# Optimization experiments

Measured on AMD Instinct MI355X. Metric: run time of the kernel, lower is better.

Reference implementation:

```python
import jax, jax.numpy as jnp
import numpy as np

L1, L2, B, D1, D2, HEADS, M = 1024, 1024, 8, 512, 1024, 16, 1024
DPH = M // HEADS  # 64


def setup_inputs() -> dict:
    key = jax.random.key(0)
    ks = jax.random.split(key, 10)
    w = lambda k, shp: jax.random.normal(k, shp, jnp.float32) * 0.02
    z = lambda n: jnp.zeros((n,), jnp.float32)
    return {
        "ctx_1": jax.random.normal(ks[0], (L1, B, D1), jnp.float32),
        "ctx_2": jax.random.normal(ks[1], (L2, B, D2), jnp.float32),
        "Wk1": w(ks[2], (M, D1)), "bk1": z(M),
        "Wv1": w(ks[3], (M, D1)), "bv1": z(M),
        "Wk2": w(ks[4], (M, D2)), "bk2": z(M),
        "Wv2": w(ks[5], (M, D2)), "bv2": z(M),
        "Wf12": w(ks[6], (M, M)), "bf12": z(M),
        "Wf21": w(ks[7], (M, M)), "bf21": z(M),
    }


def _shape_heads(x):
    # [L, B, M] -> [B, H, L, dph]
    L, Bs, _ = x.shape
    return x.reshape(L, Bs, HEADS, DPH).transpose(1, 2, 0, 3)


def _unshape(x):
    # [B, H, L, dph] -> [L, B, M]
    Bs, Hn, L, d = x.shape
    return x.transpose(2, 0, 1, 3).reshape(L, Bs, Hn * d)


def reference(ctx_1, ctx_2, Wk1, bk1, Wv1, bv1, Wk2, bk2, Wv2, bv2,
              Wf12, bf12, Wf21, bf21):
    k1 = _shape_heads(ctx_1 @ Wk1.T + bk1)  # [B,H,L1,d]
    v1 = _shape_heads(ctx_1 @ Wv1.T + bv1)  # [B,H,L1,d]
    k2 = _shape_heads(ctx_2 @ Wk2.T + bk2)  # [B,H,L2,d]
    v2 = _shape_heads(ctx_2 @ Wv2.T + bv2)  # [B,H,L2,d]

    # scores: key_2 @ key_1^T -> [B, H, L2, L1]
    scores = jnp.einsum('bhqd,bhkd->bhqk', k2, k1)

    # direction 1 -> 2: softmax over dim=2 (the L2 axis), then AV with value_1
    dist_1_to_2 = jax.nn.softmax(scores, axis=2)
    context_1_to_2 = jnp.einsum('bhqk,bhkd->bhqd', dist_1_to_2, v1)  # [B,H,L2,d]
    context_1_to_2 = _unshape(context_1_to_2) @ Wf12.T + bf12        # [L2,B,M]

    # direction 2 -> 1: softmax over dim=1 (the head axis), transpose, AV with value_2
    dist_2_to_1 = jax.nn.softmax(scores, axis=1)
    context_2_to_1 = jnp.einsum('bhqk,bhqd->bhkd', dist_2_to_1, v2)  # [B,H,L1,d]
    context_2_to_1 = _unshape(context_2_to_1) @ Wf21.T + bf21        # [L1,B,M]

    return (context_2_to_1, context_1_to_2)
```

## Files before the change

kernel.cpp:

```cpp
#include <hip/hip_runtime.h>
#include <hip/hip_bf16.h>

constexpr int LQ  = 1024;
constexpr int BN  = 8;
constexpr int D1N = 512;
constexpr int D2N = 1024;
constexpr int HN  = 16;
constexpr int MN  = 1024;
constexpr int DPH = 64;

typedef __attribute__((ext_vector_type(8)))  short bf16x8;
typedef __attribute__((ext_vector_type(2)))  float f32x2;
typedef __attribute__((ext_vector_type(4)))  float f32x4;
typedef __attribute__((ext_vector_type(16))) float f32x16;

__device__ __forceinline__ unsigned short f2bf(float f) {
  unsigned u = __float_as_uint(f);
  u += 0x7FFFu + ((u >> 16) & 1u);
  return (unsigned short)(u >> 16);
}
__device__ __forceinline__ float bf2f(unsigned short u) {
  return __uint_as_float(((unsigned)u) << 16);
}
__device__ __forceinline__ float rcpf(float x) {
  float r;
  asm("v_rcp_f32 %0, %1" : "=v"(r) : "v"(x));
  return r;
}

__device__ __forceinline__ f32x4 mfma16(bf16x8 a, bf16x8 b, f32x4 c) {
  return __builtin_amdgcn_mfma_f32_16x16x32_bf16(a, b, c, 0, 0, 0);
}
__device__ __forceinline__ f32x16 mfma32(bf16x8 a, bf16x8 b, f32x16 c) {
  return __builtin_amdgcn_mfma_f32_32x32x16_bf16(a, b, c, 0, 0, 0);
}
__device__ __forceinline__ f32x16 zero16() {
  f32x16 z;
#pragma unroll
  for (int i = 0; i < 16; ++i) z[i] = 0.f;
  return z;
}

__device__ __forceinline__ unsigned cvtpk(float lo, float hi) {
  unsigned r;
  asm("v_cvt_pk_bf16_f32 %0, %1, %2" : "=v"(r) : "v"(lo), "v"(hi));
  return r;
}

__device__ __forceinline__ bf16x8 pfrag(const float* p) {
  unsigned x0 = cvtpk(p[0], p[1]), y0 = cvtpk(p[4], p[5]);
  unsigned x1 = cvtpk(p[2], p[3]), y1 = cvtpk(p[6], p[7]);
  asm volatile("v_permlane32_swap_b32 %0, %1" : "+v"(x0), "+v"(y0));
  asm volatile("v_permlane32_swap_b32 %0, %1" : "+v"(x1), "+v"(y1));
  union { unsigned u[4]; bf16x8 v; } r;
  r.u[0] = x0; r.u[1] = x1; r.u[2] = y0; r.u[3] = y1;
  return r.v;
}

__device__ __forceinline__ bf16x8 pack8(f32x4 p0, f32x4 p1) {
  bf16x8 o;
  o[0] = (short)f2bf(p0[0]); o[1] = (short)f2bf(p0[1]);
  o[2] = (short)f2bf(p0[2]); o[3] = (short)f2bf(p0[3]);
  o[4] = (short)f2bf(p1[0]); o[5] = (short)f2bf(p1[1]);
  o[6] = (short)f2bf(p1[2]); o[7] = (short)f2bf(p1[3]);
  return o;
}

__global__ __launch_bounds__(256) void cvt_kernel(const float* __restrict__ src,
                                                  unsigned short* __restrict__ dst,
                                                  int n8) {
  int i = blockIdx.x * blockDim.x + threadIdx.x;
  if (i >= n8) return;
  const f32x4* s = (const f32x4*)src;
  f32x4 x = s[2 * i], y = s[2 * i + 1];
  ((bf16x8*)dst)[i] = pack8(x, y);
}

template <int K, int MODE>
__global__ __launch_bounds__(256) void gemm_kernel(const unsigned short* __restrict__ A,
                                                   const unsigned short* __restrict__ W,
                                                   const float* __restrict__ bias,
                                                   void* __restrict__ outp) {
  __shared__ unsigned short As[128 * 40], Bs[128 * 40];
  const int tid = threadIdx.x, wave = tid >> 6, lane = tid & 63;
  const int lg = lane >> 4, lm = lane & 15;
  const int rowb = blockIdx.x * 128, colb = blockIdx.y * 128;
  const int wrow = (wave >> 1) * 64, wcol = (wave & 1) * 64;
  const int sr = tid >> 1, sh = (tid & 1) * 16;
  const unsigned short* Arow = A + (size_t)(rowb + sr) * K + sh;
  const unsigned short* Wrow = W + (size_t)(colb + sr) * K + sh;

  f32x4 acc[4][4];
#pragma unroll
  for (int i = 0; i < 4; ++i)
#pragma unroll
    for (int j = 0; j < 4; ++j) acc[i][j] = (f32x4){0.f, 0.f, 0.f, 0.f};

  for (int kk = 0; kk < K; kk += 32) {
    bf16x8 a0 = *(const bf16x8*)(Arow + kk);
    bf16x8 a1 = *(const bf16x8*)(Arow + kk + 8);
    bf16x8 b0 = *(const bf16x8*)(Wrow + kk);
    bf16x8 b1 = *(const bf16x8*)(Wrow + kk + 8);
    __syncthreads();
    *(bf16x8*)&As[sr * 40 + sh] = a0;
    *(bf16x8*)&As[sr * 40 + sh + 8] = a1;
    *(bf16x8*)&Bs[sr * 40 + sh] = b0;
    *(bf16x8*)&Bs[sr * 40 + sh + 8] = b1;
    __syncthreads();
    bf16x8 af[4], wf[4];
#pragma unroll
    for (int i = 0; i < 4; ++i) af[i] = *(const bf16x8*)&As[(wrow + i * 16 + lm) * 40 + lg * 8];
#pragma unroll
    for (int j = 0; j < 4; ++j) wf[j] = *(const bf16x8*)&Bs[(wcol + j * 16 + lm) * 40 + lg * 8];
#pragma unroll
    for (int i = 0; i < 4; ++i)
#pragma unroll
      for (int j = 0; j < 4; ++j) acc[i][j] = mfma16(af[i], wf[j], acc[i][j]);
  }

#pragma unroll
  for (int j = 0; j < 4; ++j) {
    int col = colb + wcol + j * 16 + lm;
    float bs = bias[col];
#pragma unroll
    for (int i = 0; i < 4; ++i) {
#pragma unroll
      for (int r = 0; r < 4; ++r) {
        int row = rowb + wrow + i * 16 + lg * 4 + r;
        float v = acc[i][j][r] + bs;
        if (MODE == 0) {
          int l = row >> 3, bb = row & 7, h = col >> 6, d = col & 63;
          ((unsigned short*)outp)[(((size_t)(bb * HN + h)) * LQ + l) * DPH + d] = f2bf(v);
        } else {
          ((float*)outp)[(size_t)row * MN + col] = v;
        }
      }
    }
  }
}

__global__ __launch_bounds__(256) void transpose_kernel(const unsigned short* __restrict__ V,
                                                        unsigned short* __restrict__ VT,
                                                        const float* __restrict__ scale) {
  __shared__ unsigned short t[64][72];
  int bh = blockIdx.y, l0 = blockIdx.x * 64;
  int tid = threadIdx.x;
  int r = tid >> 2, c0 = (tid & 3) * 16;
  const unsigned short* src = V + ((size_t)bh * LQ + l0 + r) * DPH + c0;
  bf16x8 v0 = *(const bf16x8*)(src);
  bf16x8 v1 = *(const bf16x8*)(src + 8);
  if (scale) {
    float sc = scale[(size_t)bh * LQ + l0 + r];
#pragma unroll
    for (int j = 0; j < 8; ++j) {
      v0[j] = (short)f2bf(bf2f((unsigned short)v0[j]) * sc);
      v1[j] = (short)f2bf(bf2f((unsigned short)v1[j]) * sc);
    }
  }
  *(bf16x8*)&t[r][c0] = v0;
  *(bf16x8*)&t[r][c0 + 8] = v1;
  __syncthreads();
  int d = tid >> 2, lc = (tid & 3) * 16;
  bf16x8 o0, o1;
#pragma unroll
  for (int j = 0; j < 8; ++j) {
    o0[j] = (short)t[lc + j][d];
    o1[j] = (short)t[lc + 8 + j][d];
  }
  unsigned short* dst = VT + ((size_t)bh * DPH + d) * LQ + l0 + lc;
  *(bf16x8*)dst = o0;
  *(bf16x8*)(dst + 8) = o1;
}

__global__ __launch_bounds__(256) void col_reduce_kernel(const unsigned short* __restrict__ K1p,
                                                         const unsigned short* __restrict__ K2p,
                                                         float* __restrict__ inv_colsum) {
  int bh = blockIdx.y, kb = blockIdx.x * 128;
  int wave = threadIdx.x >> 6, lane = threadIdx.x & 63, l31 = lane & 31, sg = lane >> 5;
  int k0w = kb + wave * 32;
  const unsigned short* k1 = K1p + (size_t)bh * LQ * DPH;
  const unsigned short* k2 = K2p + (size_t)bh * LQ * DPH;
  bf16x8 bk[4];
#pragma unroll
  for (int i = 0; i < 4; ++i)
    bk[i] = *(const bf16x8*)(k1 + (size_t)(k0w + l31) * DPH + i * 16 + sg * 8);
  float tot = 0.f;
  for (int q0 = 0; q0 < LQ; q0 += 32) {
    bf16x8 aq[4];
#pragma unroll
    for (int i = 0; i < 4; ++i)
      aq[i] = *(const bf16x8*)(k2 + (size_t)(q0 + l31) * DPH + i * 16 + sg * 8);
    f32x16 cs = zero16();
#pragma unroll
    for (int i = 0; i < 4; ++i) cs = mfma32(aq[i], bk[i], cs);
#pragma unroll
    for (int r = 0; r < 16; ++r) tot += __expf(cs[r]);
  }
  tot += __shfl_xor(tot, 32);
  if (lane < 32) inv_colsum[(size_t)bh * LQ + k0w + lane] = 1.0f / tot;
}

__global__ __launch_bounds__(256) void ctx12_kernel(const unsigned short* __restrict__ K1p,
                                                    const unsigned short* __restrict__ K2p,
                                                    const unsigned short* __restrict__ V1Ts,
                                                    unsigned short* __restrict__ c12) {
  int bh = blockIdx.y, b = bh >> 4, h = bh & 15;
  int wave = threadIdx.x >> 6, lane = threadIdx.x & 63, l31 = lane & 31, sg = lane >> 5;
  int q0 = blockIdx.x * 128 + wave * 32;
  const unsigned short* k1 = K1p + (size_t)bh * LQ * DPH;
  const unsigned short* k2 = K2p + (size_t)bh * LQ * DPH;
  const unsigned short* vt = V1Ts + (size_t)bh * DPH * LQ;

  bf16x8 bq[4];
#pragma unroll
  for (int i = 0; i < 4; ++i)
    bq[i] = *(const bf16x8*)(k2 + (size_t)(q0 + l31) * DPH + i * 16 + sg * 8);

  f32x16 acc0 = zero16(), acc1 = zero16();
  for (int k0 = 0; k0 < LQ; k0 += 32) {
    bf16x8 ak[4];
#pragma unroll
    for (int i = 0; i < 4; ++i)
      ak[i] = *(const bf16x8*)(k1 + (size_t)(k0 + l31) * DPH + i * 16 + sg * 8);
    f32x16 cs = zero16();
#pragma unroll
    for (int i = 0; i < 4; ++i) cs = mfma32(ak[i], bq[i], cs);
    float p[16];
#pragma unroll
    for (int r = 0; r < 16; ++r) p[r] = __expf(cs[r]);
    bf16x8 pa0 = pfrag(p), pa1 = pfrag(p + 8);
    bf16x8 v00 = *(const bf16x8*)(vt + (size_t)l31 * LQ + k0 + sg * 8);
    bf16x8 v01 = *(const bf16x8*)(vt + (size_t)l31 * LQ + k0 + 16 + sg * 8);
    bf16x8 v10 = *(const bf16x8*)(vt + (size_t)(32 + l31) * LQ + k0 + sg * 8);
    bf16x8 v11 = *(const bf16x8*)(vt + (size_t)(32 + l31) * LQ + k0 + 16 + sg * 8);
    acc0 = mfma32(pa0, v00, acc0);
    acc0 = mfma32(pa1, v01, acc0);
    acc1 = mfma32(pa0, v10, acc1);
    acc1 = mfma32(pa1, v11, acc1);
  }
#pragma unroll
  for (int r = 0; r < 16; ++r) {
    int q = q0 + (r & 3) + 8 * (r >> 2) + 4 * sg;
    size_t base = ((size_t)q * BN + b) * MN + h * 64;
    c12[base + l31] = f2bf(acc0[r]);
    c12[base + 32 + l31] = f2bf(acc1[r]);
  }
}

__global__ __launch_bounds__(1024) void ctx21_fused_kernel(const unsigned short* __restrict__ K1p,
                                                           const unsigned short* __restrict__ K2p,
                                                           const unsigned short* __restrict__ V2T,
                                                           unsigned short* __restrict__ c21) {
  constexpr int SP = 34;
  constexpr int WS = 32 * SP;
  __shared__ float strip[16 * WS];
  __shared__ float tot[WS];
  const int b = blockIdx.x, kb = blockIdx.y;
  const int tid = threadIdx.x, wave = tid >> 6, lane = tid & 63;
  const int l31 = lane & 31, sg = lane >> 5;
  const int h = wave, bh = b * HN + h;
  const int k0 = kb * 32;
  const unsigned short* k1 = K1p + (size_t)bh * LQ * DPH;
  const unsigned short* k2 = K2p + (size_t)bh * LQ * DPH;
  const unsigned short* vt = V2T + (size_t)bh * DPH * LQ;
  float* mystrip = &strip[wave * WS];

  const int bk_ = tid & 31, bq2 = (tid >> 5) * 2;

  bf16x8 bk[4];
#pragma unroll
  for (int i = 0; i < 4; ++i)
    bk[i] = *(const bf16x8*)(k1 + (size_t)(k0 + l31) * DPH + i * 16 + sg * 8);

  f32x16 acc0 = zero16(), acc1 = zero16();

  for (int t = 0; t < LQ / 32; ++t) {
    const int q0 = t * 32;
    bf16x8 aq[4];
#pragma unroll
    for (int i = 0; i < 4; ++i)
      aq[i] = *(const bf16x8*)(k2 + (size_t)(q0 + l31) * DPH + i * 16 + sg * 8);
    f32x16 cs = zero16();
#pragma unroll
    for (int i = 0; i < 4; ++i) cs = mfma32(aq[i], bk[i], cs);
    float pex[16];
#pragma unroll
    for (int r = 0; r < 16; ++r) pex[r] = __expf(cs[r]);
#pragma unroll
    for (int g = 0; g < 4; ++g) {
      int qb = g * 8 + 4 * sg;
      *(f32x2*)&mystrip[l31 * SP + qb]     = (f32x2){pex[4 * g],     pex[4 * g + 1]};
      *(f32x2*)&mystrip[l31 * SP + qb + 2] = (f32x2){pex[4 * g + 2], pex[4 * g + 3]};
    }
    bf16x8 v00 = *(const bf16x8*)(vt + (size_t)l31 * LQ + q0 + sg * 8);
    bf16x8 v01 = *(const bf16x8*)(vt + (size_t)l31 * LQ + q0 + 16 + sg * 8);
    bf16x8 v10 = *(const bf16x8*)(vt + (size_t)(32 + l31) * LQ + q0 + sg * 8);
    bf16x8 v11 = *(const bf16x8*)(vt + (size_t)(32 + l31) * LQ + q0 + 16 + sg * 8);
    __syncthreads();
    if (tid < 512) {
      int off = bk_ * SP + bq2;
      f32x2 s = *(const f32x2*)&strip[off];
#pragma unroll
      for (int w = 1; w < 16; ++w) {
        f32x2 v = *(const f32x2*)&strip[w * WS + off];
        s.x += v.x; s.y += v.y;
      }
      f32x2 rc; rc.x = rcpf(s.x); rc.y = rcpf(s.y);
      *(f32x2*)&tot[off] = rc;
    }
    __syncthreads();
    float p8a[8], p8b[8];
#pragma unroll
    for (int g = 0; g < 4; ++g) {
      int qb = g * 8 + 4 * sg;
      f32x2 t0 = *(const f32x2*)&tot[l31 * SP + qb];
      f32x2 t1 = *(const f32x2*)&tot[l31 * SP + qb + 2];
      float* dstp = (g < 2) ? &p8a[(g & 1) * 4] : &p8b[(g & 1) * 4];
      dstp[0] = pex[4 * g]     * t0.x;
      dstp[1] = pex[4 * g + 1] * t0.y;
      dstp[2] = pex[4 * g + 2] * t1.x;
      dstp[3] = pex[4 * g + 3] * t1.y;
    }
    bf16x8 pa0 = pfrag(p8a), pa1 = pfrag(p8b);
    acc0 = mfma32(pa0, v00, acc0);
    acc0 = mfma32(pa1, v01, acc0);
    acc1 = mfma32(pa0, v10, acc1);
    acc1 = mfma32(pa1, v11, acc1);
  }
#pragma unroll
  for (int r = 0; r < 16; ++r) {
    int k = k0 + (r & 3) + 8 * (r >> 2) + 4 * sg;
    size_t base = ((size_t)k * BN + b) * MN + h * 64;
    c21[base + l31] = f2bf(acc0[r]);
    c21[base + 32 + l31] = f2bf(acc1[r]);
  }
}

extern "C" void kernel_launch(void* const* d_in, const int* in_sizes, int n_in,
                              void* d_out, int out_size, void* d_ws, size_t ws_size,
                              hipStream_t stream) {
  const float* ctx1 = (const float*)d_in[0];
  const float* ctx2 = (const float*)d_in[1];
  const float* Wk1 = (const float*)d_in[2];  const float* bk1 = (const float*)d_in[3];
  const float* Wv1 = (const float*)d_in[4];  const float* bv1 = (const float*)d_in[5];
  const float* Wk2 = (const float*)d_in[6];  const float* bk2 = (const float*)d_in[7];
  const float* Wv2 = (const float*)d_in[8];  const float* bv2 = (const float*)d_in[9];
  const float* Wf12 = (const float*)d_in[10]; const float* bf12 = (const float*)d_in[11];
  const float* Wf21 = (const float*)d_in[12]; const float* bf21 = (const float*)d_in[13];

  char* ws = (char*)d_ws;
  size_t off = 0;
  auto alloc = [&](size_t bytes) {
    void* p = ws + off;
    off += (bytes + 255) & ~(size_t)255;
    return p;
  };
  const size_t KV_BYTES = (size_t)BN * HN * LQ * DPH * 2;

  unsigned short* ctx1b = (unsigned short*)alloc((size_t)LQ * BN * D1N * 2);
  unsigned short* ctx2b = (unsigned short*)alloc((size_t)LQ * BN * D2N * 2);
  unsigned short* wk1b = (unsigned short*)alloc((size_t)MN * D1N * 2);
  unsigned short* wv1b = (unsigned short*)alloc((size_t)MN * D1N * 2);
  unsigned short* wk2b = (unsigned short*)alloc((size_t)MN * D2N * 2);
  unsigned short* wv2b = (unsigned short*)alloc((size_t)MN * D2N * 2);
  unsigned short* wf12b = (unsigned short*)alloc((size_t)MN * MN * 2);
  unsigned short* wf21b = (unsigned short*)alloc((size_t)MN * MN * 2);
  unsigned short* K1buf = (unsigned short*)alloc(KV_BYTES);
  unsigned short* K2buf = (unsigned short*)alloc(KV_BYTES);
  unsigned short* V1T = (unsigned short*)alloc(KV_BYTES);
  unsigned short* V2T = (unsigned short*)alloc(KV_BYTES);
  float* invcs = (float*)alloc((size_t)BN * HN * LQ * 4);
  unsigned short* c12 = (unsigned short*)alloc(KV_BYTES);
  unsigned short* c21 = (unsigned short*)alloc(KV_BYTES);
  unsigned short* V1tmp = c12;
  unsigned short* V2tmp = c21;

  auto cvt = [&](const float* s, unsigned short* d, int n) {
    int n8 = n / 8;
    cvt_kernel<<<(n8 + 255) / 256, 256, 0, stream>>>(s, d, n8);
  };
  cvt(ctx1, ctx1b, LQ * BN * D1N);
  cvt(ctx2, ctx2b, LQ * BN * D2N);
  cvt(Wk1, wk1b, MN * D1N);
  cvt(Wv1, wv1b, MN * D1N);
  cvt(Wk2, wk2b, MN * D2N);
  cvt(Wv2, wv2b, MN * D2N);
  cvt(Wf12, wf12b, MN * MN);
  cvt(Wf21, wf21b, MN * MN);

  dim3 gp(64, 8);
  gemm_kernel<D1N, 0><<<gp, 256, 0, stream>>>(ctx1b, wk1b, bk1, K1buf);
  gemm_kernel<D1N, 0><<<gp, 256, 0, stream>>>(ctx1b, wv1b, bv1, V1tmp);
  gemm_kernel<D2N, 0><<<gp, 256, 0, stream>>>(ctx2b, wk2b, bk2, K2buf);
  gemm_kernel<D2N, 0><<<gp, 256, 0, stream>>>(ctx2b, wv2b, bv2, V2tmp);

  col_reduce_kernel<<<dim3(LQ / 128, BN * HN), 256, 0, stream>>>(K1buf, K2buf, invcs);
  dim3 gt(LQ / 64, BN * HN);
  transpose_kernel<<<gt, 256, 0, stream>>>(V1tmp, V1T, invcs);
  transpose_kernel<<<gt, 256, 0, stream>>>(V2tmp, V2T, nullptr);

  ctx12_kernel<<<dim3(LQ / 128, BN * HN), 256, 0, stream>>>(K1buf, K2buf, V1T, c12);
  ctx21_fused_kernel<<<dim3(BN, LQ / 32), 1024, 0, stream>>>(K1buf, K2buf, V2T, c21);

  float* out0 = (float*)d_out;
  float* out1 = out0 + (size_t)LQ * BN * MN;
  gemm_kernel<MN, 2><<<gp, 256, 0, stream>>>(c21, wf21b, bf21, out0);
  gemm_kernel<MN, 2><<<gp, 256, 0, stream>>>(c12, wf12b, bf12, out1);
}
```

Before: 514.8 us.

## Replace LDS GEMM with direct-load 32x32 MFMA GEMM, fuse fp32 input conversion

Replaces the LDS-tiled 16x16 MFMA GEMM with a kernel that loads A and W fragments straight from global memory into 32x32x16 MFMAs, with no shared memory or barriers. The K and V projections for each context are merged into one launch, and the fp32 activations are converted to bf16 inside the GEMM, which removes two conversion kernels and their workspace buffers. The ctx21 kernel now prefetches the next K2 tile while the current scores are computed, and uses a lighter LDS-only barrier. The trade-off is that each wave rereads operands with no LDS reuse, which puts more load on L2 and global memory bandwidth.

```diff
diff --git a/kernel.cpp b/kernel.cpp
--- a/kernel.cpp
+++ b/kernel.cpp
@@ -28,9 +28,6 @@
   return r;
 }
 
-__device__ __forceinline__ f32x4 mfma16(bf16x8 a, bf16x8 b, f32x4 c) {
-  return __builtin_amdgcn_mfma_f32_16x16x32_bf16(a, b, c, 0, 0, 0);
-}
 __device__ __forceinline__ f32x16 mfma32(bf16x8 a, bf16x8 b, f32x16 c) {
   return __builtin_amdgcn_mfma_f32_32x32x16_bf16(a, b, c, 0, 0, 0);
 }
@@ -45,6 +42,11 @@
   unsigned r;
   asm("v_cvt_pk_bf16_f32 %0, %1, %2" : "=v"(r) : "v"(lo), "v"(hi));
   return r;
+}
+
+__device__ __forceinline__ void lds_barrier() {
+  asm volatile("s_waitcnt lgkmcnt(0)" ::: "memory");
+  __builtin_amdgcn_s_barrier();
 }
 
 __device__ __forceinline__ bf16x8 pfrag(const float* p) {
@@ -65,6 +67,12 @@
   o[6] = (short)f2bf(p1[2]); o[7] = (short)f2bf(p1[3]);
   return o;
 }
+__device__ __forceinline__ bf16x8 pack8q(f32x4 lo, f32x4 hi) {
+  union { unsigned u[4]; bf16x8 v; } r;
+  r.u[0] = cvtpk(lo[0], lo[1]); r.u[1] = cvtpk(lo[2], lo[3]);
+  r.u[2] = cvtpk(hi[0], hi[1]); r.u[3] = cvtpk(hi[2], hi[3]);
+  return r.v;
+}
 
 __global__ __launch_bounds__(256) void cvt_kernel(const float* __restrict__ src,
                                                   unsigned short* __restrict__ dst,
@@ -76,58 +84,71 @@
   ((bf16x8*)dst)[i] = pack8(x, y);
 }
 
-template <int K, int MODE>
-__global__ __launch_bounds__(256) void gemm_kernel(const unsigned short* __restrict__ A,
-                                                   const unsigned short* __restrict__ W,
-                                                   const float* __restrict__ bias,
-                                                   void* __restrict__ outp) {
-  __shared__ unsigned short As[128 * 40], Bs[128 * 40];
-  const int tid = threadIdx.x, wave = tid >> 6, lane = tid & 63;
-  const int lg = lane >> 4, lm = lane & 15;
-  const int rowb = blockIdx.x * 128, colb = blockIdx.y * 128;
-  const int wrow = (wave >> 1) * 64, wcol = (wave & 1) * 64;
-  const int sr = tid >> 1, sh = (tid & 1) * 16;
-  const unsigned short* Arow = A + (size_t)(rowb + sr) * K + sh;
-  const unsigned short* Wrow = W + (size_t)(colb + sr) * K + sh;
-
-  f32x4 acc[4][4];
-#pragma unroll
-  for (int i = 0; i < 4; ++i)
-#pragma unroll
-    for (int j = 0; j < 4; ++j) acc[i][j] = (f32x4){0.f, 0.f, 0.f, 0.f};
-
+template <int K, int MODE, bool AF32>
+__global__ __launch_bounds__(256) void gemm32_kernel(
+    const void* __restrict__ Ap,
+    const unsigned short* __restrict__ W0, const unsigned short* __restrict__ W1,
+    const float* __restrict__ b0, const float* __restrict__ b1,
+    void* __restrict__ o0, void* __restrict__ o1) {
+  const int wave = threadIdx.x >> 6, lane = threadIdx.x & 63;
+  const int l31 = lane & 31, sg = lane >> 5;
+  const int wr = wave >> 1, wc = wave & 1;
+  const int rowb = blockIdx.x * 128 + wr * 64;
+  const int sel = blockIdx.y >> 3;
+  const int colb = (blockIdx.y & 7) * 128 + wc * 64;
+  const unsigned short* W = sel ? W1 : W0;
+  const float* bias = sel ? b1 : b0;
+  void* outp = sel ? o1 : o0;
+
+  const unsigned short* Wr0 = W + (size_t)(colb + l31) * K + sg * 8;
+  const unsigned short* Wr1 = W + (size_t)(colb + 32 + l31) * K + sg * 8;
+
+  f32x16 acc00 = zero16(), acc01 = zero16(), acc10 = zero16(), acc11 = zero16();
+
+#pragma unroll 2
   for (int kk = 0; kk < K; kk += 32) {
-    bf16x8 a0 = *(const bf16x8*)(Arow + kk);
-    bf16x8 a1 = *(const bf16x8*)(Arow + kk + 8);
-    bf16x8 b0 = *(const bf16x8*)(Wrow + kk);
-    bf16x8 b1 = *(const bf16x8*)(Wrow + kk + 8);
-    __syncthreads();
-    *(bf16x8*)&As[sr * 40 + sh] = a0;
-    *(bf16x8*)&As[sr * 40 + sh + 8] = a1;
-    *(bf16x8*)&Bs[sr * 40 + sh] = b0;
-    *(bf16x8*)&Bs[sr * 40 + sh + 8] = b1;
-    __syncthreads();
-    bf16x8 af[4], wf[4];
-#pragma unroll
-    for (int i = 0; i < 4; ++i) af[i] = *(const bf16x8*)&As[(wrow + i * 16 + lm) * 40 + lg * 8];
-#pragma unroll
-    for (int j = 0; j < 4; ++j) wf[j] = *(const bf16x8*)&Bs[(wcol + j * 16 + lm) * 40 + lg * 8];
-#pragma unroll
-    for (int i = 0; i < 4; ++i)
-#pragma unroll
-      for (int j = 0; j < 4; ++j) acc[i][j] = mfma16(af[i], wf[j], acc[i][j]);
-  }
-
-#pragma unroll
-  for (int j = 0; j < 4; ++j) {
-    int col = colb + wcol + j * 16 + lm;
+    bf16x8 a0k0, a0k1, a1k0, a1k1;
+    if (AF32) {
+      const float* Af = (const float*)Ap;
+      const float* b0p = Af + (size_t)(rowb + l31) * K + kk + sg * 8;
+      const float* b1p = Af + (size_t)(rowb + 32 + l31) * K + kk + sg * 8;
+      a0k0 = pack8q(*(const f32x4*)b0p,        *(const f32x4*)(b0p + 4));
+      a0k1 = pack8q(*(const f32x4*)(b0p + 16), *(const f32x4*)(b0p + 20));
+      a1k0 = pack8q(*(const f32x4*)b1p,        *(const f32x4*)(b1p + 4));
+      a1k1 = pack8q(*(const f32x4*)(b1p + 16), *(const f32x4*)(b1p + 20));
+    } else {
+      const unsigned short* Ab = (const unsigned short*)Ap;
+      const unsigned short* b0p = Ab + (size_t)(rowb + l31) * K + kk + sg * 8;
+      const unsigned short* b1p = Ab + (size_t)(rowb + 32 + l31) * K + kk + sg * 8;
+      a0k0 = *(const bf16x8*)b0p;  a0k1 = *(const bf16x8*)(b0p + 16);
+      a1k0 = *(const bf16x8*)b1p;  a1k1 = *(const bf16x8*)(b1p + 16);
+    }
+    bf16x8 w0k0 = *(const bf16x8*)(Wr0 + kk);
+    bf16x8 w0k1 = *(const bf16x8*)(Wr0 + kk + 16);
+    bf16x8 w1k0 = *(const bf16x8*)(Wr1 + kk);
+    bf16x8 w1k1 = *(const bf16x8*)(Wr1 + kk + 16);
+    acc00 = mfma32(a0k0, w0k0, acc00);
+    acc01 = mfma32(a0k0, w1k0, acc01);
+    acc10 = mfma32(a1k0, w0k0, acc10);
+    acc11 = mfma32(a1k0, w1k0, acc11);
+    acc00 = mfma32(a0k1, w0k1, acc00);
+    acc01 = mfma32(a0k1, w1k1, acc01);
+    acc10 = mfma32(a1k1, w0k1, acc10);
+    acc11 = mfma32(a1k1, w1k1, acc11);
+  }
+
+  const f32x16* accs[2][2] = {{&acc00, &acc01}, {&acc10, &acc11}};
+#pragma unroll
+  for (int j = 0; j < 2; ++j) {
+    int col = colb + 32 * j + l31;
     float bs = bias[col];
 #pragma unroll
-    for (int i = 0; i < 4; ++i) {
-#pragma unroll
-      for (int r = 0; r < 4; ++r) {
-        int row = rowb + wrow + i * 16 + lg * 4 + r;
-        float v = acc[i][j][r] + bs;
+    for (int i = 0; i < 2; ++i) {
+      const f32x16& a = *accs[i][j];
+#pragma unroll
+      for (int r = 0; r < 16; ++r) {
+        int row = rowb + 32 * i + (r & 3) + 8 * (r >> 2) + 4 * sg;
+        float v = a[r] + bs;
         if (MODE == 0) {
           int l = row >> 3, bb = row & 7, h = col >> 6, d = col & 63;
           ((unsigned short*)outp)[(((size_t)(bb * HN + h)) * LQ + l) * DPH + d] = f2bf(v);
@@ -272,17 +293,22 @@
   for (int i = 0; i < 4; ++i)
     bk[i] = *(const bf16x8*)(k1 + (size_t)(k0 + l31) * DPH + i * 16 + sg * 8);
 
+  bf16x8 aq[4];
+#pragma unroll
+  for (int i = 0; i < 4; ++i)
+    aq[i] = *(const bf16x8*)(k2 + (size_t)(l31) * DPH + i * 16 + sg * 8);
+
   f32x16 acc0 = zero16(), acc1 = zero16();
 
   for (int t = 0; t < LQ / 32; ++t) {
     const int q0 = t * 32;
-    bf16x8 aq[4];
+    f32x16 cs = zero16();
+#pragma unroll
+    for (int i = 0; i < 4; ++i) cs = mfma32(aq[i], bk[i], cs);
+    const int qn = ((t + 1) & 31) * 32;
 #pragma unroll
     for (int i = 0; i < 4; ++i)
-      aq[i] = *(const bf16x8*)(k2 + (size_t)(q0 + l31) * DPH + i * 16 + sg * 8);
-    f32x16 cs = zero16();
-#pragma unroll
-    for (int i = 0; i < 4; ++i) cs = mfma32(aq[i], bk[i], cs);
+      aq[i] = *(const bf16x8*)(k2 + (size_t)(qn + l31) * DPH + i * 16 + sg * 8);
     float pex[16];
 #pragma unroll
     for (int r = 0; r < 16; ++r) pex[r] = __expf(cs[r]);
@@ -296,7 +322,7 @@
     bf16x8 v01 = *(const bf16x8*)(vt + (size_t)l31 * LQ + q0 + 16 + sg * 8);
     bf16x8 v10 = *(const bf16x8*)(vt + (size_t)(32 + l31) * LQ + q0 + sg * 8);
     bf16x8 v11 = *(const bf16x8*)(vt + (size_t)(32 + l31) * LQ + q0 + 16 + sg * 8);
-    __syncthreads();
+    lds_barrier();
     if (tid < 512) {
       int off = bk_ * SP + bq2;
       f32x2 s = *(const f32x2*)&strip[off];
@@ -308,7 +334,7 @@
       f32x2 rc; rc.x = rcpf(s.x); rc.y = rcpf(s.y);
       *(f32x2*)&tot[off] = rc;
     }
-    __syncthreads();
+    lds_barrier();
     float p8a[8], p8b[8];
 #pragma unroll
     for (int g = 0; g < 4; ++g) {
@@ -357,8 +383,6 @@
   };
   const size_t KV_BYTES = (size_t)BN * HN * LQ * DPH * 2;
 
-  unsigned short* ctx1b = (unsigned short*)alloc((size_t)LQ * BN * D1N * 2);
-  unsigned short* ctx2b = (unsigned short*)alloc((size_t)LQ * BN * D2N * 2);
   unsigned short* wk1b = (unsigned short*)alloc((size_t)MN * D1N * 2);
   unsigned short* wv1b = (unsigned short*)alloc((size_t)MN * D1N * 2);
   unsigned short* wk2b = (unsigned short*)alloc((size_t)MN * D2N * 2);
@@ -379,8 +403,6 @@
     int n8 = n / 8;
     cvt_kernel<<<(n8 + 255) / 256, 256, 0, stream>>>(s, d, n8);
   };
-  cvt(ctx1, ctx1b, LQ * BN * D1N);
-  cvt(ctx2, ctx2b, LQ * BN * D2N);
   cvt(Wk1, wk1b, MN * D1N);
   cvt(Wv1, wv1b, MN * D1N);
   cvt(Wk2, wk2b, MN * D2N);
@@ -388,11 +410,10 @@
   cvt(Wf12, wf12b, MN * MN);
   cvt(Wf21, wf21b, MN * MN);
 
-  dim3 gp(64, 8);
-  gemm_kernel<D1N, 0><<<gp, 256, 0, stream>>>(ctx1b, wk1b, bk1, K1buf);
-  gemm_kernel<D1N, 0><<<gp, 256, 0, stream>>>(ctx1b, wv1b, bv1, V1tmp);
-  gemm_kernel<D2N, 0><<<gp, 256, 0, stream>>>(ctx2b, wk2b, bk2, K2buf);
-  gemm_kernel<D2N, 0><<<gp, 256, 0, stream>>>(ctx2b, wv2b, bv2, V2tmp);
+  gemm32_kernel<D1N, 0, true><<<dim3(64, 16), 256, 0, stream>>>(
+      ctx1, wk1b, wv1b, bk1, bv1, K1buf, V1tmp);
+  gemm32_kernel<D2N, 0, true><<<dim3(64, 16), 256, 0, stream>>>(
+      ctx2, wk2b, wv2b, bk2, bv2, K2buf, V2tmp);
 
   col_reduce_kernel<<<dim3(LQ / 128, BN * HN), 256, 0, stream>>>(K1buf, K2buf, invcs);
   dim3 gt(LQ / 64, BN * HN);
@@ -404,6 +425,8 @@
 
   float* out0 = (float*)d_out;
   float* out1 = out0 + (size_t)LQ * BN * MN;
-  gemm_kernel<MN, 2><<<gp, 256, 0, stream>>>(c21, wf21b, bf21, out0);
-  gemm_kernel<MN, 2><<<gp, 256, 0, stream>>>(c12, wf12b, bf12, out1);
-}
+  gemm32_kernel<MN, 2, false><<<dim3(64, 8), 256, 0, stream>>>(
+      c21, wf21b, nullptr, bf21, nullptr, out0, nullptr);
+  gemm32_kernel<MN, 2, false><<<dim3(64, 8), 256, 0, stream>>>(
+      c12, wf12b, nullptr, bf12, nullptr, out1, nullptr);
+}
```

Result: slower. 734.8 us (+42.7%).
